# Kernel tuning notes

Measured on AMD Instinct MI355X. Metric: run time of the kernel, lower is better.

## Reference

```python
import jax, jax.numpy as jnp
import numpy as np


def setup_inputs() -> dict:
    key = jax.random.key(0)
    ks = jax.random.split(key, 6)
    B, E, N, F = 512, 4, 256, 64
    node = jax.random.normal(ks[0], (B, N, F), dtype=jnp.float32)
    adj = jax.random.uniform(ks[1], (B, E, N, N), dtype=jnp.float32)
    s = 1.0 / np.sqrt(F)
    W_edge = jax.random.uniform(ks[2], (E, F, F), dtype=jnp.float32, minval=-s, maxval=s)
    b_edge = jax.random.uniform(ks[3], (E, F), dtype=jnp.float32, minval=-s, maxval=s)
    W_add = jax.random.uniform(ks[4], (F, F), dtype=jnp.float32, minval=-s, maxval=s)
    b_add = jax.random.uniform(ks[5], (F,), dtype=jnp.float32, minval=-s, maxval=s)
    return {"node": node, "adj": adj, "W_edge": W_edge, "b_edge": b_edge,
            "W_add": W_add, "b_add": b_add}


def reference(node, adj, W_edge, b_edge, W_add, b_add):
    # per-edge-type linear: [B,N,F_in] x [E,F_in,F_out] -> [B,E,N,F_out]
    hidden = jnp.einsum('bnf,efg->beng', node, W_edge) + b_edge[None, :, None, :]
    # adjacency-weighted aggregation per edge type: [B,E,N,N] @ [B,E,N,F_out]
    msg = jnp.einsum('benm,bemg->beng', adj, hidden)
    # sum over edge types + residual linear (dropout=0, activation=None)
    out = jnp.sum(msg, axis=1) + node @ W_add + b_add
    return out
```

## Files before the change

### kernel.cpp

```cpp
#include <hip/hip_runtime.h>

typedef __attribute__((ext_vector_type(8))) short short8;
typedef __attribute__((ext_vector_type(4))) float f32x4;

#define MFMA16(a, b, c) __builtin_amdgcn_mfma_f32_16x16x32_bf16((a), (b), (c), 0, 0, 0)

static __device__ inline short f2bf(float x) {
    union { float f; unsigned u; } v;
    v.f = x;
    unsigned r = v.u + 0x7fffu + ((v.u >> 16) & 1u);
    return (short)(r >> 16);
}

__global__ __launch_bounds__(256, 2) void gconv_kernel(
    const float* __restrict__ node,
    const float* __restrict__ adj,
    const float* __restrict__ W_edge,
    const float* __restrict__ b_edge,
    const float* __restrict__ W_add,
    const float* __restrict__ b_add,
    float* __restrict__ out)
{
    constexpr int N = 256, F = 64, E = 4;

    __shared__ short node_bf[N][F + 8];
    __shared__ short hiddenT[F][N + 8];
    __shared__ short wT[F][F + 8];
    const int b    = blockIdx.x;
    const int t    = threadIdx.x;
    const int lane = t & 63;
    const int w    = t >> 6;
    const int col  = lane & 15;
    const int kq   = lane >> 4;

    const float* nodeB = node + (size_t)b * (N * F);
    #pragma unroll
    for (int i = 0; i < 16; ++i) {
        int idx = i * 1024 + t * 4;
        float4 v = *(const float4*)(nodeB + idx);
        int r = idx >> 6, c = idx & 63;
        short4 s;
        s.x = f2bf(v.x); s.y = f2bf(v.y); s.z = f2bf(v.z); s.w = f2bf(v.w);
        *(short4*)&node_bf[r][c] = s;
    }
    #pragma unroll
    for (int i = 0; i < 16; ++i) {
        int idx = i * 256 + t;
        wT[idx & 63][idx >> 6] = f2bf(W_add[idx]);
    }
    __syncthreads();

    f32x4 acc[4][4];
    {
        const f32x4 zf = {0.f, 0.f, 0.f, 0.f};
        #pragma unroll
        for (int rt = 0; rt < 4; ++rt)
            #pragma unroll
            for (int ct = 0; ct < 4; ++ct)
                acc[rt][ct] = zf;
        #pragma unroll
        for (int ks = 0; ks < 2; ++ks) {
            short8 afr[4], bfr[4];
            #pragma unroll
            for (int rt = 0; rt < 4; ++rt)
                afr[rt] = *(const short8*)&node_bf[64 * w + 16 * rt + col][32 * ks + 8 * kq];
            #pragma unroll
            for (int ct = 0; ct < 4; ++ct)
                bfr[ct] = *(const short8*)&wT[16 * ct + col][32 * ks + 8 * kq];
            #pragma unroll
            for (int rt = 0; rt < 4; ++rt)
                #pragma unroll
                for (int ct = 0; ct < 4; ++ct)
                    acc[rt][ct] = MFMA16(afr[rt], bfr[ct], acc[rt][ct]);
        }
    }
    __syncthreads();

    for (int e = 0; e < E; ++e) {
        const float* We = W_edge + e * (F * F);
        #pragma unroll
        for (int i = 0; i < 16; ++i) {
            int idx = i * 256 + t;
            wT[idx & 63][idx >> 6] = f2bf(We[idx]);
        }
        __syncthreads();

        #pragma unroll
        for (int rt = 0; rt < 4; ++rt) {
            short8 a0 = *(const short8*)&node_bf[64 * w + 16 * rt + col][8 * kq];
            short8 a1 = *(const short8*)&node_bf[64 * w + 16 * rt + col][32 + 8 * kq];
            #pragma unroll
            for (int ct = 0; ct < 4; ++ct) {
                short8 b0 = *(const short8*)&wT[16 * ct + col][8 * kq];
                short8 b1 = *(const short8*)&wT[16 * ct + col][32 + 8 * kq];
                f32x4 h = {0.f, 0.f, 0.f, 0.f};
                h = MFMA16(a0, b0, h);
                h = MFMA16(a1, b1, h);
                float bias = b_edge[e * 64 + 16 * ct + col];
                short4 s;
                s.x = f2bf(h.x + bias); s.y = f2bf(h.y + bias);
                s.z = f2bf(h.z + bias); s.w = f2bf(h.w + bias);
                *(short4*)&hiddenT[16 * ct + col][64 * w + 16 * rt + 4 * kq] = s;
            }
        }
        __syncthreads();

        const float* adjBase = adj + ((size_t)(b * 4 + e)) * (N * N);
        #pragma unroll 2
        for (int ks = 0; ks < 8; ++ks) {
            const int k0 = ks * 32 + 8 * kq;
            short8 afrag[4];
            #pragma unroll
            for (int rt = 0; rt < 4; ++rt) {
                const float* p = adjBase + (64 * w + 16 * rt + col) * 256 + k0;
                float4 v0 = *(const float4*)p;
                float4 v1 = *(const float4*)(p + 4);
                short8 a;
                a[0] = f2bf(v0.x); a[1] = f2bf(v0.y); a[2] = f2bf(v0.z); a[3] = f2bf(v0.w);
                a[4] = f2bf(v1.x); a[5] = f2bf(v1.y); a[6] = f2bf(v1.z); a[7] = f2bf(v1.w);
                afrag[rt] = a;
            }
            short8 bfrag[4];
            #pragma unroll
            for (int ct = 0; ct < 4; ++ct)
                bfrag[ct] = *(const short8*)&hiddenT[16 * ct + col][ks * 32 + 8 * kq];
            #pragma unroll
            for (int rt = 0; rt < 4; ++rt)
                #pragma unroll
                for (int ct = 0; ct < 4; ++ct)
                    acc[rt][ct] = MFMA16(afrag[rt], bfrag[ct], acc[rt][ct]);
        }
        __syncthreads();
    }

    float* outB = out + (size_t)b * (N * F);
    #pragma unroll
    for (int ct = 0; ct < 4; ++ct) {
        float bias = b_add[16 * ct + col];
        #pragma unroll
        for (int rt = 0; rt < 4; ++rt) {
            int row = 64 * w + 16 * rt + 4 * kq;
            #pragma unroll
            for (int r = 0; r < 4; ++r)
                outB[(size_t)(row + r) * 64 + 16 * ct + col] = acc[rt][ct][r] + bias;
        }
    }
}

extern "C" void kernel_launch(void* const* d_in, const int* in_sizes, int n_in,
                              void* d_out, int out_size, void* d_ws, size_t ws_size,
                              hipStream_t stream) {
    const float* node   = (const float*)d_in[0];
    const float* adj    = (const float*)d_in[1];
    const float* W_edge = (const float*)d_in[2];
    const float* b_edge = (const float*)d_in[3];
    const float* W_add  = (const float*)d_in[4];
    const float* b_add  = (const float*)d_in[5];
    float* out = (float*)d_out;

    gconv_kernel<<<dim3(512), dim3(256), 0, stream>>>(
        node, adj, W_edge, b_edge, W_add, b_add, out);
}
```

Baseline: 715.7 us.

## Stage adjacency tiles through LDS with coalesced loads; keep node fragments in registers

Adjacency is now loaded cooperatively in 256x64 column tiles with fully coalesced float4 row reads, converted to bf16 and written to LDS. MFMA A-fragments are then read from LDS rather than gathered directly from strided global rows. Node bf16 fragments are held in registers instead of a shared array, which frees LDS for the adjacency tile. The cost is two extra barriers per tile and serialized load-then-compute with no double buffering.

```diff
diff --git a/kernel.cpp b/kernel.cpp
--- a/kernel.cpp
+++ b/kernel.cpp
@@ -11,6 +11,11 @@
     unsigned r = v.u + 0x7fffu + ((v.u >> 16) & 1u);
     return (short)(r >> 16);
 }
+static __device__ inline short4 f2bf4(float4 v) {
+    short4 s;
+    s.x = f2bf(v.x); s.y = f2bf(v.y); s.z = f2bf(v.z); s.w = f2bf(v.w);
+    return s;
+}
 
 __global__ __launch_bounds__(256, 2) void gconv_kernel(
     const float* __restrict__ node,
@@ -21,11 +26,11 @@
     const float* __restrict__ b_add,
     float* __restrict__ out)
 {
-    constexpr int N = 256, F = 64, E = 4;
+    constexpr int E = 4;
 
-    __shared__ short node_bf[N][F + 8];
-    __shared__ short hiddenT[F][N + 8];
-    __shared__ short wT[F][F + 8];
+    __shared__ short adjL[256][72];
+    __shared__ short hiddenT[64][264];
+    __shared__ short wT[64][72];
     const int b    = blockIdx.x;
     const int t    = threadIdx.x;
     const int lane = t & 63;
@@ -33,16 +38,21 @@
     const int col  = lane & 15;
     const int kq   = lane >> 4;
 
-    const float* nodeB = node + (size_t)b * (N * F);
+    const float* nodeB = node + (size_t)b * (256 * 64);
+    short8 anode[4][2];
     #pragma unroll
-    for (int i = 0; i < 16; ++i) {
-        int idx = i * 1024 + t * 4;
-        float4 v = *(const float4*)(nodeB + idx);
-        int r = idx >> 6, c = idx & 63;
-        short4 s;
-        s.x = f2bf(v.x); s.y = f2bf(v.y); s.z = f2bf(v.z); s.w = f2bf(v.w);
-        *(short4*)&node_bf[r][c] = s;
-    }
+    for (int rt = 0; rt < 4; ++rt)
+        #pragma unroll
+        for (int h = 0; h < 2; ++h) {
+            const float* p = nodeB + (64 * w + 16 * rt + col) * 64 + 32 * h + 8 * kq;
+            float4 v0 = *(const float4*)p;
+            float4 v1 = *(const float4*)(p + 4);
+            short8 a;
+            a[0] = f2bf(v0.x); a[1] = f2bf(v0.y); a[2] = f2bf(v0.z); a[3] = f2bf(v0.w);
+            a[4] = f2bf(v1.x); a[5] = f2bf(v1.y); a[6] = f2bf(v1.z); a[7] = f2bf(v1.w);
+            anode[rt][h] = a;
+        }
+
     #pragma unroll
     for (int i = 0; i < 16; ++i) {
         int idx = i * 256 + t;
@@ -59,25 +69,22 @@
             for (int ct = 0; ct < 4; ++ct)
                 acc[rt][ct] = zf;
         #pragma unroll
-        for (int ks = 0; ks < 2; ++ks) {
-            short8 afr[4], bfr[4];
-            #pragma unroll
-            for (int rt = 0; rt < 4; ++rt)
-                afr[rt] = *(const short8*)&node_bf[64 * w + 16 * rt + col][32 * ks + 8 * kq];
+        for (int h = 0; h < 2; ++h) {
+            short8 bfr[4];
             #pragma unroll
             for (int ct = 0; ct < 4; ++ct)
-                bfr[ct] = *(const short8*)&wT[16 * ct + col][32 * ks + 8 * kq];
+                bfr[ct] = *(const short8*)&wT[16 * ct + col][32 * h + 8 * kq];
             #pragma unroll
             for (int rt = 0; rt < 4; ++rt)
                 #pragma unroll
                 for (int ct = 0; ct < 4; ++ct)
-                    acc[rt][ct] = MFMA16(afr[rt], bfr[ct], acc[rt][ct]);
+                    acc[rt][ct] = MFMA16(anode[rt][h], bfr[ct], acc[rt][ct]);
         }
     }
     __syncthreads();
 
     for (int e = 0; e < E; ++e) {
-        const float* We = W_edge + e * (F * F);
+        const float* We = W_edge + e * (64 * 64);
         #pragma unroll
         for (int i = 0; i < 16; ++i) {
             int idx = i * 256 + t;
@@ -87,15 +94,13 @@
 
         #pragma unroll
         for (int rt = 0; rt < 4; ++rt) {
-            short8 a0 = *(const short8*)&node_bf[64 * w + 16 * rt + col][8 * kq];
-            short8 a1 = *(const short8*)&node_bf[64 * w + 16 * rt + col][32 + 8 * kq];
             #pragma unroll
             for (int ct = 0; ct < 4; ++ct) {
                 short8 b0 = *(const short8*)&wT[16 * ct + col][8 * kq];
                 short8 b1 = *(const short8*)&wT[16 * ct + col][32 + 8 * kq];
                 f32x4 h = {0.f, 0.f, 0.f, 0.f};
-                h = MFMA16(a0, b0, h);
-                h = MFMA16(a1, b1, h);
+                h = MFMA16(anode[rt][0], b0, h);
+                h = MFMA16(anode[rt][1], b1, h);
                 float bias = b_edge[e * 64 + 16 * ct + col];
                 short4 s;
                 s.x = f2bf(h.x + bias); s.y = f2bf(h.y + bias);
@@ -105,35 +110,41 @@
         }
         __syncthreads();
 
-        const float* adjBase = adj + ((size_t)(b * 4 + e)) * (N * N);
-        #pragma unroll 2
-        for (int ks = 0; ks < 8; ++ks) {
-            const int k0 = ks * 32 + 8 * kq;
-            short8 afrag[4];
+        const float* adjE = adj + ((size_t)(b * 4 + e)) * (256 * 256);
+        for (int kt = 0; kt < 4; ++kt) {
+            {
+                const int c4  = t & 15;
+                const int r0  = t >> 4;
+                const float* base = adjE + kt * 64 + c4 * 4;
+                #pragma unroll
+                for (int i = 0; i < 16; ++i) {
+                    int row = i * 16 + r0;
+                    float4 v = *(const float4*)(base + row * 256);
+                    *(short4*)&adjL[row][c4 * 4] = f2bf4(v);
+                }
+            }
+            __syncthreads();
+
             #pragma unroll
-            for (int rt = 0; rt < 4; ++rt) {
-                const float* p = adjBase + (64 * w + 16 * rt + col) * 256 + k0;
-                float4 v0 = *(const float4*)p;
-                float4 v1 = *(const float4*)(p + 4);
-                short8 a;
-                a[0] = f2bf(v0.x); a[1] = f2bf(v0.y); a[2] = f2bf(v0.z); a[3] = f2bf(v0.w);
-                a[4] = f2bf(v1.x); a[5] = f2bf(v1.y); a[6] = f2bf(v1.z); a[7] = f2bf(v1.w);
-                afrag[rt] = a;
-            }
-            short8 bfrag[4];
-            #pragma unroll
-            for (int ct = 0; ct < 4; ++ct)
-                bfrag[ct] = *(const short8*)&hiddenT[16 * ct + col][ks * 32 + 8 * kq];
-            #pragma unroll
-            for (int rt = 0; rt < 4; ++rt)
+            for (int ks2 = 0; ks2 < 2; ++ks2) {
+                short8 afrag[4], bfrag[4];
+                #pragma unroll
+                for (int rt = 0; rt < 4; ++rt)
+                    afrag[rt] = *(const short8*)&adjL[64 * w + 16 * rt + col][32 * ks2 + 8 * kq];
                 #pragma unroll
                 for (int ct = 0; ct < 4; ++ct)
-                    acc[rt][ct] = MFMA16(afrag[rt], bfrag[ct], acc[rt][ct]);
+                    bfrag[ct] = *(const short8*)&hiddenT[16 * ct + col][kt * 64 + 32 * ks2 + 8 * kq];
+                #pragma unroll
+                for (int rt = 0; rt < 4; ++rt)
+                    #pragma unroll
+                    for (int ct = 0; ct < 4; ++ct)
+                        acc[rt][ct] = MFMA16(afrag[rt], bfrag[ct], acc[rt][ct]);
+            }
+            __syncthreads();
         }
-        __syncthreads();
     }
 
-    float* outB = out + (size_t)b * (N * F);
+    float* outB = out + (size_t)b * (256 * 64);
     #pragma unroll
     for (int ct = 0; ct < 4; ++ct) {
         float bias = b_add[16 * ct + col];
```

Result: no change. 712.5 us (-0.5%).
